# Kernel optimization log

Measured on AMD Instinct MI355X. Metric: run time of the kernel, lower is better.

## Reference

```python
import jax, jax.numpy as jnp
import numpy as np

L, B, Q, D = 6, 2, 300, 256  # levels, batch, num queries, embed dim


def setup_inputs() -> dict:
    key = jax.random.key(0)
    ks = jax.random.split(key, 20)
    s = 1.0 / np.sqrt(D)
    s2 = 1.0 / np.sqrt(2 * D)
    inp = {
        "hs": jax.random.normal(ks[0], (L, B, Q, D), jnp.float32),
        # per-level proj_q / proj_k (Linear(D, D) cloned L times)
        "Wq": jax.random.uniform(ks[1], (L, D, D), jnp.float32, -s, s),
        "bq": jax.random.uniform(ks[2], (L, D), jnp.float32, -s, s),
        "Wk": jax.random.uniform(ks[3], (L, D, D), jnp.float32, -s, s),
        "bk": jax.random.uniform(ks[4], (L, D), jnp.float32, -s, s),
        # final subject/object projections on hs[-1]
        "Wsub": jax.random.uniform(ks[5], (D, D), jnp.float32, -s, s),
        "bsub": jax.random.uniform(ks[6], (D,), jnp.float32, -s, s),
        "Wobj": jax.random.uniform(ks[7], (D, D), jnp.float32, -s, s),
        "bobj": jax.random.uniform(ks[8], (D,), jnp.float32, -s, s),
        # gate: Linear(2D, 1)
        "Wg": jax.random.uniform(ks[9], (2 * D, 1), jnp.float32, -s2, s2),
        "bg": jax.random.uniform(ks[10], (1,), jnp.float32, -s2, s2),
        # MLPHEAD: 2D -> D -> D -> 1
        "W1": jax.random.uniform(ks[11], (2 * D, D), jnp.float32, -s2, s2),
        "b1": jax.random.uniform(ks[12], (D,), jnp.float32, -s2, s2),
        "W2": jax.random.uniform(ks[13], (D, D), jnp.float32, -s, s),
        "b2": jax.random.uniform(ks[14], (D,), jnp.float32, -s, s),
        "W3": jax.random.uniform(ks[15], (D, 1), jnp.float32, -s, s),
        "b3": jax.random.uniform(ks[16], (1,), jnp.float32, -s, s),
    }
    return inp


def reference(hs, Wq, bq, Wk, bk, Wsub, bsub, Wobj, bobj, Wg, bg, W1, b1, W2, b2, W3, b3):
    l, b, q, d = hs.shape
    # per-level projections: [L, B, Q, D]
    Qs = jnp.einsum('lbqd,lde->lbqe', hs, Wq) + bq[:, None, None, :]
    Ks = jnp.einsum('lbqd,lde->lbqe', hs, Wk) + bk[:, None, None, :]
    # extra (L+1)-th level from final sub/obj projections of hs[-1]
    sub = hs[-1] @ Wsub + bsub  # [B, Q, D]
    obj = hs[-1] @ Wobj + bobj
    Q_all = jnp.concatenate([Qs, sub[None]], axis=0)  # [L+1, B, Q, D]
    K_all = jnp.concatenate([Ks, obj[None]], axis=0)
    # gate logit for pair (i, j) at level m = wa.q_m[i] + wb.k_m[j] + bg,
    # identical math to sigmoid(Linear(cat([q_i, k_j]))) without materializing
    # the [B, Q, Q, L+1, 2D] broadcast tensor.
    wa, wb = Wg[:d, 0], Wg[d:, 0]
    gq = jnp.einsum('lbqd,d->lbq', Q_all, wa)  # [L+1, B, Q]
    gk = jnp.einsum('lbqd,d->lbq', K_all, wb)
    gate = jax.nn.sigmoid(gq[:, :, :, None] + gk[:, :, None, :] + bg[0])  # [L+1, B, Qi, Qj]
    # gated sum over levels; query half depends on i, key half on j
    out_q = jnp.einsum('lbij,lbid->bijd', gate, Q_all)  # [B, Q, Q, D]
    out_k = jnp.einsum('lbij,lbjd->bijd', gate, K_all)
    gated = jnp.concatenate([out_q, out_k], axis=-1)  # [B, Q, Q, 2D]
    # rel predictor MLP: 2D -> D -> D -> 1
    x = jax.nn.relu(gated @ W1 + b1)
    x = jax.nn.relu(x @ W2 + b2)
    pred = (x @ W3 + b3)[..., 0]  # [B, Q, Q]
    pred_rel = jnp.broadcast_to(pred[None], (l,) + pred.shape)  # [L, B, Q, Q]
    return pred_rel
```

## Files before the change

### kernel.cpp

```cpp
#include <hip/hip_runtime.h>


typedef _Float16 half8 __attribute__((ext_vector_type(8)));
typedef _Float16 half4v __attribute__((ext_vector_type(4)));
typedef float floatx4 __attribute__((ext_vector_type(4)));

#define MFMA16(a, b, c) __builtin_amdgcn_mfma_f32_16x16x32_f16((a), (b), (c), 0, 0, 0)

__global__ __launch_bounds__(256) void k_wprep(
    const float* __restrict__ Wq, const float* __restrict__ Wk,
    const float* __restrict__ Wsub, const float* __restrict__ Wobj,
    const float* __restrict__ W1, _Float16* __restrict__ WT)
{
    int eid = blockIdx.x * 256 + threadIdx.x;
    int mat = eid >> 13;
    int rem = eid & 8191;
    int tileid = rem >> 6;
    int lane = rem & 63;
    const float* src;
    if      (mat < 6)  src = Wq + mat * 65536;
    else if (mat < 12) src = Wk + (mat - 6) * 65536;
    else if (mat == 12) src = Wsub;
    else if (mat == 13) src = Wobj;
    else if (mat == 14) src = W1;
    else               src = W1 + 65536;
    int nb = tileid >> 3, kb = tileid & 7;
    int n = nb * 16 + (lane & 15);
    int k = kb * 32 + (lane >> 4) * 8;
    half8 h;
    #pragma unroll
    for (int j = 0; j < 8; ++j) h[j] = (_Float16)src[(k + j) * 256 + n];
    *(half8*)(WT + mat * 65536 + tileid * 512 + lane * 8) = h;
}

__global__ __launch_bounds__(256) void k_projpq(
    const float* __restrict__ hs, _Float16* __restrict__ WT,
    const float* __restrict__ bq, const float* __restrict__ bk,
    const float* __restrict__ bsub, const float* __restrict__ bobj,
    const float* __restrict__ Wg, const float* __restrict__ W2,
    _Float16* __restrict__ PQt, _Float16* __restrict__ PKt,
    float* __restrict__ g_ws)
{
    int t = threadIdx.x;
    if (blockIdx.x >= 532) {
        int eid = (blockIdx.x - 532) * 256 + t;
        int tileid = eid >> 6, lane = eid & 63;
        int nb = tileid >> 3, kb = tileid & 7;
        int n = nb * 16 + (lane & 15);
        int k = kb * 32 + (lane >> 4) * 8;
        half8 h;
        #pragma unroll
        for (int j = 0; j < 8; ++j) h[j] = (_Float16)W2[(k + j) * 256 + n];
        *(half8*)(WT + 16 * 65536 + tileid * 512 + lane * 8) = h;
        return;
    }

    __shared__ __align__(16) _Float16 Ah[16][264];
    __shared__ __align__(16) _Float16 Xb[16][264];

    int lane = t & 63, wv = t >> 6;
    int mr = lane & 15, hf = lane >> 4;
    int u = blockIdx.x;
    int s = u / 19, rt = u - s * 19;
    int m0 = rt * 16;
    int qk = s & 1, rr = s >> 1;
    int l = rr % 7, b = rr / 7;
    int hs_l = (l < 6) ? l : 5;
    const float* src = hs + (hs_l * 2 + b) * 76800;
    int projmat = (l < 6) ? (qk * 6 + l) : (12 + qk);
    const _Float16* WprojT = WT + projmat * 65536;
    const _Float16* W1hT = WT + (14 + qk) * 65536;
    const float* bias = (l < 6) ? ((qk ? bk : bq) + l * 256) : (qk ? bobj : bsub);
    _Float16* dstP = qk ? PKt : PQt;
    const float* wvec = Wg + qk * 256;
    float* gdst = g_ws + qk * 4200 + (l * 2 + b) * 300;

    {
        int row = t >> 4, qt = t & 15;
        int m = m0 + row; if (m > 299) m = 299;
        const float* pp = src + m * 256 + qt * 16;
        #pragma unroll
        for (int i = 0; i < 4; ++i) {
            float4 v = *(const float4*)(pp + 4 * i);
            half4v h;
            h[0] = (_Float16)v.x; h[1] = (_Float16)v.y;
            h[2] = (_Float16)v.z; h[3] = (_Float16)v.w;
            *(half4v*)&Ah[row][qt * 16 + 4 * i] = h;
        }
    }
    __syncthreads();

    floatx4 acc[4];
    #pragma unroll
    for (int i = 0; i < 4; ++i) acc[i] = floatx4{0.f, 0.f, 0.f, 0.f};
    #pragma unroll
    for (int ks = 0; ks < 8; ++ks) {
        half8 bfr = *(const half8*)&Ah[mr][ks * 32 + hf * 8];
        #pragma unroll
        for (int mt = 0; mt < 4; ++mt) {
            half8 afr = *(const half8*)(WprojT + (((wv * 4 + mt) * 8 + ks) << 9) + lane * 8);
            acc[mt] = MFMA16(afr, bfr, acc[mt]);
        }
    }
    #pragma unroll
    for (int mt = 0; mt < 4; ++mt) {
        int n0 = wv * 64 + mt * 16 + hf * 4;
        float4 bb = *(const float4*)&bias[n0];
        float bv[4] = {bb.x, bb.y, bb.z, bb.w};
        half4v h;
        #pragma unroll
        for (int u2 = 0; u2 < 4; ++u2) h[u2] = (_Float16)(acc[mt][u2] + bv[u2]);
        *(half4v*)&Xb[mr][n0] = h;
    }
    __syncthreads();

    {
        int row = t >> 4, qt = t & 15;
        half8 x0 = *(const half8*)&Xb[row][qt * 16];
        half8 x1 = *(const half8*)&Xb[row][qt * 16 + 8];
        const float* wp = wvec + qt * 16;
        float sum = 0.f;
        #pragma unroll
        for (int i = 0; i < 8; ++i) sum += (float)x0[i] * wp[i];
        #pragma unroll
        for (int i = 0; i < 8; ++i) sum += (float)x1[i] * wp[8 + i];
        sum += __shfl_xor(sum, 1);
        sum += __shfl_xor(sum, 2);
        sum += __shfl_xor(sum, 4);
        sum += __shfl_xor(sum, 8);
        int m = m0 + row;
        if (qt == 0 && m < 300) gdst[m] = sum;
    }

    floatx4 acc2[4];
    #pragma unroll
    for (int i = 0; i < 4; ++i) acc2[i] = floatx4{0.f, 0.f, 0.f, 0.f};
    #pragma unroll
    for (int ks = 0; ks < 8; ++ks) {
        half8 bfr = *(const half8*)&Xb[mr][ks * 32 + hf * 8];
        #pragma unroll
        for (int mt = 0; mt < 4; ++mt) {
            half8 afr = *(const half8*)(W1hT + (((wv * 4 + mt) * 8 + ks) << 9) + lane * 8);
            acc2[mt] = MFMA16(afr, bfr, acc2[mt]);
        }
    }
    #pragma unroll
    for (int mt = 0; mt < 4; ++mt) {
        int n0 = wv * 64 + mt * 16 + hf * 4;
        half4v h;
        #pragma unroll
        for (int u2 = 0; u2 < 4; ++u2) h[u2] = (_Float16)acc2[mt][u2];
        *(half4v*)&Ah[mr][n0] = h;
    }
    __syncthreads();

    #pragma unroll
    for (int z = 0; z < 2; ++z) {
        int it = rt * 2 + z;
        int n = t;
        half8 h;
        #pragma unroll
        for (int io = 0; io < 8; ++io) h[io] = Ah[z * 8 + io][n];
        *(half8*)(dstP + ((size_t)((b * 38 + it) * 7 + l) * 256 + n) * 8) = h;
    }
}

__global__ __launch_bounds__(256, 4) void k_fused(
    const _Float16* __restrict__ PQt, const _Float16* __restrict__ PKt,
    const float* __restrict__ g_ws, const float* __restrict__ b1,
    const _Float16* __restrict__ W2T, const float* __restrict__ b2,
    const float* __restrict__ W3, const float* __restrict__ b3,
    const float* __restrict__ bg, float* __restrict__ out)
{
    union SM {
        _Float16 Pt[256][72];
        _Float16 X[64][264];
    };
    __shared__ __align__(16) SM sm;
    __shared__ float gate[7][64];

    int t = threadIdx.x, lane = t & 63, wv = t >> 6;
    int mr = lane & 15, hf = lane >> 4;
    int bid = blockIdx.x;
    int b = bid / 1444, rem = bid - b * 1444;
    int it = rem / 38, jt = rem - it * 38;
    int i0 = it * 8, j0 = jt * 8;

    const _Float16* baseQ = PQt + ((size_t)((b * 38 + it) * 7) * 256 + t) * 8;
    const _Float16* baseK = PKt + ((size_t)((b * 38 + jt) * 7) * 256 + t) * 8;
    half8 pq[7], pk[7];
    #pragma unroll
    for (int l = 0; l < 7; ++l) pq[l] = *(const half8*)(baseQ + l * 2048);
    #pragma unroll
    for (int l = 0; l < 7; ++l) pk[l] = *(const half8*)(baseK + l * 2048);

    float bg0 = bg[0];
    for (int task = t; task < 448; task += 256) {
        int l = task >> 6, row = task & 63;
        int i = i0 + (row >> 3); if (i > 299) i = 299;
        int j = j0 + (row & 7);  if (j > 299) j = 299;
        float z = g_ws[l * 600 + b * 300 + i] + g_ws[4200 + l * 600 + b * 300 + j] + bg0;
        gate[l][row] = 1.0f / (1.0f + __expf(-z));
    }

    #pragma unroll
    for (int l = 0; l < 7; ++l)
        *(half8*)&sm.Pt[t][l * 8] = pq[l];
    *(half8*)&sm.Pt[t][56] = half8{};
    __syncthreads();

    floatx4 acc1[4][4];
    #pragma unroll
    for (int i = 0; i < 4; ++i)
        #pragma unroll
        for (int j = 0; j < 4; ++j) acc1[i][j] = floatx4{0.f, 0.f, 0.f, 0.f};

    #pragma unroll
    for (int ktl = 0; ktl < 2; ++ktl) {
        int l = ktl * 4 + hf;
        half8 bfr[4];
        #pragma unroll
        for (int nt = 0; nt < 4; ++nt) {
            int r = nt * 16 + mr;
            float g = (l < 7) ? gate[l][r] : 0.f;
            _Float16 gh = (_Float16)g;
            const _Float16 hz = (_Float16)0.f;
            half8 f = {};
            f[nt * 2]     = (mr < 8)  ? gh : hz;
            f[nt * 2 + 1] = (mr >= 8) ? gh : hz;
            bfr[nt] = f;
        }
        #pragma unroll
        for (int mt = 0; mt < 4; ++mt) {
            half8 afr = *(const half8*)&sm.Pt[wv * 64 + mt * 16 + mr][ktl * 32 + hf * 8];
            #pragma unroll
            for (int nt = 0; nt < 4; ++nt)
                acc1[mt][nt] = MFMA16(afr, bfr[nt], acc1[mt][nt]);
        }
    }
    __syncthreads();

    #pragma unroll
    for (int l = 0; l < 7; ++l)
        *(half8*)&sm.Pt[t][l * 8] = pk[l];
    __syncthreads();

    #pragma unroll
    for (int ktl = 0; ktl < 2; ++ktl) {
        int l = ktl * 4 + hf;
        half8 bfr[4];
        #pragma unroll
        for (int nt = 0; nt < 4; ++nt) {
            int r = nt * 16 + mr;
            float g = (l < 7) ? gate[l][r] : 0.f;
            _Float16 gh = (_Float16)g;
            const _Float16 hz = (_Float16)0.f;
            half8 f = {};
            #pragma unroll
            for (int j = 0; j < 8; ++j)
                f[j] = (j == (mr & 7)) ? gh : hz;
            bfr[nt] = f;
        }
        #pragma unroll
        for (int mt = 0; mt < 4; ++mt) {
            half8 afr = *(const half8*)&sm.Pt[wv * 64 + mt * 16 + mr][ktl * 32 + hf * 8];
            #pragma unroll
            for (int nt = 0; nt < 4; ++nt)
                acc1[mt][nt] = MFMA16(afr, bfr[nt], acc1[mt][nt]);
        }
    }
    __syncthreads();

    #pragma unroll
    for (int mt = 0; mt < 4; ++mt) {
        int n0 = wv * 64 + mt * 16 + hf * 4;
        float4 bb = *(const float4*)&b1[n0];
        float bv[4] = {bb.x, bb.y, bb.z, bb.w};
        #pragma unroll
        for (int nt = 0; nt < 4; ++nt) {
            int r = nt * 16 + mr;
            half4v h;
            #pragma unroll
            for (int u = 0; u < 4; ++u) {
                float v = acc1[mt][nt][u] + bv[u];
                h[u] = (_Float16)(v > 0.f ? v : 0.f);
            }
            *(half4v*)&sm.X[r][n0] = h;
        }
    }
    __syncthreads();

    floatx4 acc2[4][4];
    #pragma unroll
    for (int i = 0; i < 4; ++i)
        #pragma unroll
        for (int j = 0; j < 4; ++j) acc2[i][j] = floatx4{0.f, 0.f, 0.f, 0.f};
    for (int s = 0; s < 8; ++s) {
        half8 bfr[4];
        #pragma unroll
        for (int nt = 0; nt < 4; ++nt)
            bfr[nt] = *(const half8*)&sm.X[nt * 16 + mr][s * 32 + hf * 8];
        #pragma unroll
        for (int mt = 0; mt < 4; ++mt) {
            half8 afr = *(const half8*)(W2T + (((wv * 4 + mt) * 8 + s) << 9) + lane * 8);
            #pragma unroll
            for (int nt = 0; nt < 4; ++nt)
                acc2[mt][nt] = MFMA16(afr, bfr[nt], acc2[mt][nt]);
        }
    }

    {
        float* red = &gate[0][0];
        float p[4] = {0.f, 0.f, 0.f, 0.f};
        #pragma unroll
        for (int mt = 0; mt < 4; ++mt) {
            int n0 = wv * 64 + mt * 16 + hf * 4;
            float4 bb = *(const float4*)&b2[n0];
            float4 w3 = *(const float4*)&W3[n0];
            float bv[4] = {bb.x, bb.y, bb.z, bb.w};
            float wv3[4] = {w3.x, w3.y, w3.z, w3.w};
            #pragma unroll
            for (int nt = 0; nt < 4; ++nt)
                #pragma unroll
                for (int u = 0; u < 4; ++u) {
                    float v = acc2[mt][nt][u] + bv[u];
                    v = v > 0.f ? v : 0.f;
                    p[nt] += v * wv3[u];
                }
        }
        #pragma unroll
        for (int nt = 0; nt < 4; ++nt) {
            p[nt] += __shfl_xor(p[nt], 16);
            p[nt] += __shfl_xor(p[nt], 32);
        }
        if (hf == 0) {
            #pragma unroll
            for (int nt = 0; nt < 4; ++nt)
                red[wv * 64 + nt * 16 + mr] = p[nt];
        }
        __syncthreads();
        if (t < 64) {
            float pred = red[t] + red[64 + t] + red[128 + t] + red[192 + t] + b3[0];
            int i = i0 + (t >> 3), j = j0 + (t & 7);
            if (i < 300 && j < 300) {
                int base = b * 90000 + i * 300 + j;
                #pragma unroll
                for (int lo = 0; lo < 6; ++lo) out[lo * 180000 + base] = pred;
            }
        }
    }
}

extern "C" void kernel_launch(void* const* d_in, const int* in_sizes, int n_in,
                              void* d_out, int out_size, void* d_ws, size_t ws_size,
                              hipStream_t stream) {
    (void)in_sizes; (void)n_in; (void)out_size; (void)ws_size;
    const float* hs   = (const float*)d_in[0];
    const float* Wq   = (const float*)d_in[1];
    const float* bq   = (const float*)d_in[2];
    const float* Wk   = (const float*)d_in[3];
    const float* bk   = (const float*)d_in[4];
    const float* Wsub = (const float*)d_in[5];
    const float* bsub = (const float*)d_in[6];
    const float* Wobj = (const float*)d_in[7];
    const float* bobj = (const float*)d_in[8];
    const float* Wg   = (const float*)d_in[9];
    const float* bg   = (const float*)d_in[10];
    const float* W1   = (const float*)d_in[11];
    const float* b1   = (const float*)d_in[12];
    const float* W2   = (const float*)d_in[13];
    const float* b2   = (const float*)d_in[14];
    const float* W3   = (const float*)d_in[15];
    const float* b3   = (const float*)d_in[16];

    char* ws = (char*)d_ws;
    float* g_ws   = (float*)ws;
    _Float16* WT  = (_Float16*)(ws + 33600);
    _Float16* PQt = WT + 17 * 65536;
    _Float16* PKt = PQt + 1089536;

    k_wprep<<<512, 256, 0, stream>>>(Wq, Wk, Wsub, Wobj, W1, WT);
    k_projpq<<<564, 256, 0, stream>>>(hs, WT, bq, bk, bsub, bobj, Wg, W2,
                                      PQt, PKt, g_ws);
    k_fused<<<2888, 256, 0, stream>>>(PQt, PKt, g_ws, b1, WT + 16 * 65536,
                                      b2, W3, b3, bg, (float*)d_out);
}
```

Measured before the change: 145.5 us.

## Stage gate one-hot fragments in LDS and load projection tiles directly from global

The first gated-sum GEMM no longer transposes the Q/K projection tiles through shared memory. The gate values are now written once as one-hot half8 B fragments into a smaller LDS buffer. The A fragments are read straight from global memory, with the next level's tile prefetched while the current MFMAs run. This removes the Pt staging writes, two barriers and the per-fragment gate construction, and shrinks the shared-memory footprint, which may allow higher occupancy. In exchange the A fragment loads from global are less coalesced per wave, and the reduction scratch now reuses the X buffer behind an extra barrier.

```diff
diff --git a/kernel.cpp b/kernel.cpp
--- a/kernel.cpp
+++ b/kernel.cpp
@@ -172,12 +172,11 @@
     const float* __restrict__ W3, const float* __restrict__ b3,
     const float* __restrict__ bg, float* __restrict__ out)
 {
-    union SM {
-        _Float16 Pt[256][72];
+    union SMu {
+        _Float16 B[2][64][72];
         _Float16 X[64][264];
     };
-    __shared__ __align__(16) SM sm;
-    __shared__ float gate[7][64];
+    __shared__ __align__(16) SMu sm;
 
     int t = threadIdx.x, lane = t & 63, wv = t >> 6;
     int mr = lane & 15, hf = lane >> 4;
@@ -186,27 +185,47 @@
     int it = rem / 38, jt = rem - it * 38;
     int i0 = it * 8, j0 = jt * 8;
 
-    const _Float16* baseQ = PQt + ((size_t)((b * 38 + it) * 7) * 256 + t) * 8;
-    const _Float16* baseK = PKt + ((size_t)((b * 38 + jt) * 7) * 256 + t) * 8;
-    half8 pq[7], pk[7];
-    #pragma unroll
-    for (int l = 0; l < 7; ++l) pq[l] = *(const half8*)(baseQ + l * 2048);
-    #pragma unroll
-    for (int l = 0; l < 7; ++l) pk[l] = *(const half8*)(baseK + l * 2048);
-
+    const _Float16* tQ = PQt + (size_t)((b * 38 + it) * 7) * 2048;
+    const _Float16* tK = PKt + (size_t)((b * 38 + jt) * 7) * 2048;
+    int l0 = hf;
+    int l1 = (hf == 3) ? 6 : 4 + hf;
+    int nb8[4];
+    #pragma unroll
+    for (int mt = 0; mt < 4; ++mt) nb8[mt] = (wv * 64 + mt * 16 + mr) * 8;
+
+    half8 aA[4];
+    #pragma unroll
+    for (int mt = 0; mt < 4; ++mt)
+        aA[mt] = *(const half8*)(tQ + l0 * 2048 + nb8[mt]);
+
+    _Float16* Bf = &sm.B[0][0][0];
     float bg0 = bg[0];
-    for (int task = t; task < 448; task += 256) {
-        int l = task >> 6, row = task & 63;
-        int i = i0 + (row >> 3); if (i > 299) i = 299;
-        int j = j0 + (row & 7);  if (j > 299) j = 299;
-        float z = g_ws[l * 600 + b * 300 + i] + g_ws[4200 + l * 600 + b * 300 + j] + bg0;
-        gate[l][row] = 1.0f / (1.0f + __expf(-z));
-    }
-
-    #pragma unroll
-    for (int l = 0; l < 7; ++l)
-        *(half8*)&sm.Pt[t][l * 8] = pq[l];
-    *(half8*)&sm.Pt[t][56] = half8{};
+    #pragma unroll
+    for (int half = 0; half < 2; ++half) {
+        int task = t + half * 256;
+        if (task < 448) {
+            int l = task >> 6, r = task & 63;
+            int i = i0 + (r >> 3); if (i > 299) i = 299;
+            int j = j0 + (r & 7);  if (j > 299) j = 299;
+            float z = g_ws[l * 600 + b * 300 + i]
+                    + g_ws[4200 + l * 600 + b * 300 + j] + bg0;
+            _Float16 gh = (_Float16)(1.0f / (1.0f + __expf(-z)));
+            const _Float16 hz0 = (_Float16)0.f;
+            int s0 = r >> 3, s1 = r & 7;
+            half8 f0, f1;
+            #pragma unroll
+            for (int u = 0; u < 8; ++u) {
+                f0[u] = (u == s0) ? gh : hz0;
+                f1[u] = (u == s1) ? gh : hz0;
+            }
+            *(half8*)&Bf[(size_t)r * 72 + l * 8] = f0;
+            *(half8*)&Bf[4608 + (size_t)r * 72 + l * 8] = f1;
+        } else {
+            int r = task - 448;
+            *(half8*)&Bf[(size_t)r * 72 + 56] = half8{};
+            *(half8*)&Bf[4608 + (size_t)r * 72 + 56] = half8{};
+        }
+    }
     __syncthreads();
 
     floatx4 acc1[4][4];
@@ -215,59 +234,58 @@
         #pragma unroll
         for (int j = 0; j < 4; ++j) acc1[i][j] = floatx4{0.f, 0.f, 0.f, 0.f};
 
-    #pragma unroll
-    for (int ktl = 0; ktl < 2; ++ktl) {
-        int l = ktl * 4 + hf;
+    {
         half8 bfr[4];
         #pragma unroll
-        for (int nt = 0; nt < 4; ++nt) {
-            int r = nt * 16 + mr;
-            float g = (l < 7) ? gate[l][r] : 0.f;
-            _Float16 gh = (_Float16)g;
-            const _Float16 hz = (_Float16)0.f;
-            half8 f = {};
-            f[nt * 2]     = (mr < 8)  ? gh : hz;
-            f[nt * 2 + 1] = (mr >= 8) ? gh : hz;
-            bfr[nt] = f;
-        }
-        #pragma unroll
-        for (int mt = 0; mt < 4; ++mt) {
-            half8 afr = *(const half8*)&sm.Pt[wv * 64 + mt * 16 + mr][ktl * 32 + hf * 8];
-            #pragma unroll
-            for (int nt = 0; nt < 4; ++nt)
-                acc1[mt][nt] = MFMA16(afr, bfr[nt], acc1[mt][nt]);
-        }
-    }
-    __syncthreads();
-
-    #pragma unroll
-    for (int l = 0; l < 7; ++l)
-        *(half8*)&sm.Pt[t][l * 8] = pk[l];
-    __syncthreads();
-
-    #pragma unroll
-    for (int ktl = 0; ktl < 2; ++ktl) {
-        int l = ktl * 4 + hf;
-        half8 bfr[4];
-        #pragma unroll
-        for (int nt = 0; nt < 4; ++nt) {
-            int r = nt * 16 + mr;
-            float g = (l < 7) ? gate[l][r] : 0.f;
-            _Float16 gh = (_Float16)g;
-            const _Float16 hz = (_Float16)0.f;
-            half8 f = {};
-            #pragma unroll
-            for (int j = 0; j < 8; ++j)
-                f[j] = (j == (mr & 7)) ? gh : hz;
-            bfr[nt] = f;
-        }
-        #pragma unroll
-        for (int mt = 0; mt < 4; ++mt) {
-            half8 afr = *(const half8*)&sm.Pt[wv * 64 + mt * 16 + mr][ktl * 32 + hf * 8];
-            #pragma unroll
-            for (int nt = 0; nt < 4; ++nt)
-                acc1[mt][nt] = MFMA16(afr, bfr[nt], acc1[mt][nt]);
-        }
+        for (int nt = 0; nt < 4; ++nt)
+            bfr[nt] = *(const half8*)&Bf[(size_t)(nt * 16 + mr) * 72 + hf * 8];
+        half8 aB[4];
+        #pragma unroll
+        for (int mt = 0; mt < 4; ++mt)
+            aB[mt] = *(const half8*)(tQ + l1 * 2048 + nb8[mt]);
+        #pragma unroll
+        for (int mt = 0; mt < 4; ++mt)
+            #pragma unroll
+            for (int nt = 0; nt < 4; ++nt)
+                acc1[mt][nt] = MFMA16(aA[mt], bfr[nt], acc1[mt][nt]);
+
+        half8 bfr1[4];
+        #pragma unroll
+        for (int nt = 0; nt < 4; ++nt)
+            bfr1[nt] = *(const half8*)&Bf[(size_t)(nt * 16 + mr) * 72 + 32 + hf * 8];
+        half8 aC[4];
+        #pragma unroll
+        for (int mt = 0; mt < 4; ++mt)
+            aC[mt] = *(const half8*)(tK + l0 * 2048 + nb8[mt]);
+        #pragma unroll
+        for (int mt = 0; mt < 4; ++mt)
+            #pragma unroll
+            for (int nt = 0; nt < 4; ++nt)
+                acc1[mt][nt] = MFMA16(aB[mt], bfr1[nt], acc1[mt][nt]);
+
+        half8 bfr2[4];
+        #pragma unroll
+        for (int nt = 0; nt < 4; ++nt)
+            bfr2[nt] = *(const half8*)&Bf[4608 + (size_t)(nt * 16 + mr) * 72 + hf * 8];
+        half8 aD[4];
+        #pragma unroll
+        for (int mt = 0; mt < 4; ++mt)
+            aD[mt] = *(const half8*)(tK + l1 * 2048 + nb8[mt]);
+        #pragma unroll
+        for (int mt = 0; mt < 4; ++mt)
+            #pragma unroll
+            for (int nt = 0; nt < 4; ++nt)
+                acc1[mt][nt] = MFMA16(aC[mt], bfr2[nt], acc1[mt][nt]);
+
+        half8 bfr3[4];
+        #pragma unroll
+        for (int nt = 0; nt < 4; ++nt)
+            bfr3[nt] = *(const half8*)&Bf[4608 + (size_t)(nt * 16 + mr) * 72 + 32 + hf * 8];
+        #pragma unroll
+        for (int mt = 0; mt < 4; ++mt)
+            #pragma unroll
+            for (int nt = 0; nt < 4; ++nt)
+                acc1[mt][nt] = MFMA16(aD[mt], bfr3[nt], acc1[mt][nt]);
     }
     __syncthreads();
 
@@ -310,7 +328,6 @@
     }
 
     {
-        float* red = &gate[0][0];
         float p[4] = {0.f, 0.f, 0.f, 0.f};
         #pragma unroll
         for (int mt = 0; mt < 4; ++mt) {
@@ -333,6 +350,8 @@
             p[nt] += __shfl_xor(p[nt], 16);
             p[nt] += __shfl_xor(p[nt], 32);
         }
+        __syncthreads();
+        float* red = (float*)&sm.X[0][0];
         if (hf == 0) {
             #pragma unroll
             for (int nt = 0; nt < 4; ++nt)
```

Result: no change. 146.5 us (+0.7%).
